# Optimization experiments

Hardware: AMD Instinct MI355X
Metric: run time of the kernel (lower is better)

The kernel has to match this reference:

```python
import jax, jax.numpy as jnp
import numpy as np

N_NODES = 50000
N_EDGES = 800000
IN_F = 128
OUT_F = 64
ORDER = 3


def _spmm(edge_index, edge_attr, x):
    # out[row] += edge_attr[e] * x[col]  (COO sparse @ dense)
    row, col = edge_index[0], edge_index[1]
    msgs = x[col] * edge_attr[:, None]          # [E, F] gather + scale
    return jax.ops.segment_sum(msgs, row, num_segments=N_NODES)  # scatter-add


def setup_inputs() -> dict:
    key = jax.random.key(0)
    k1, k2, k3, k4 = jax.random.split(key, 4)
    x = jax.random.normal(k1, (N_NODES, IN_F), dtype=jnp.float32)
    edge_index = jax.random.randint(k2, (2, N_EDGES), 0, N_NODES, dtype=jnp.int64)
    edge_attr = jax.random.uniform(k3, (N_EDGES,), dtype=jnp.float32)
    W = jax.random.normal(k4, (OUT_F, IN_F), dtype=jnp.float32) * (1.0 / np.sqrt(IN_F))
    b = jnp.zeros((OUT_F,), dtype=jnp.float32)
    return {"x": x, "edge_index": edge_index, "edge_attr": edge_attr, "W": W, "b": b}


def reference(x, edge_index, edge_attr, W, b):
    # output = Linear(x); then `order` rounds of spmm aggregation
    out = jnp.einsum("ni,oi->no", x, W) + b      # [N, OUT_F]
    for _ in range(ORDER):
        out = _spmm(edge_index, edge_attr, out)
    return out
```

## Files before the change

kernel.cpp:

```cpp
#include <hip/hip_runtime.h>

#define IN_F   128
#define OUT_F  64
#define GR     64
#define EPB    4096

__device__ __forceinline__ unsigned short f2bf(float f) {
    unsigned int u = __float_as_uint(f);
    u += 0x7fffu + ((u >> 16) & 1u);
    return (unsigned short)(u >> 16);
}
__device__ __forceinline__ float bf2f(unsigned short h) {
    return __uint_as_float(((unsigned int)h) << 16);
}

template <bool BF16OUT>
__global__ __launch_bounds__(256) void gemm_kernel(
    const float* __restrict__ x, const float* __restrict__ W,
    const float* __restrict__ b, void* __restrict__ outv, int N) {
    __shared__ float xs[GR][IN_F + 4];
    __shared__ float Wt[IN_F][OUT_F + 4];

    const int t = threadIdx.x;
    const int row0 = blockIdx.x * GR;

    for (int i = t; i < OUT_F * (IN_F / 4); i += 256) {
        int o = i & 63;
        int c = i >> 6;
        float4 v = ((const float4*)W)[o * (IN_F / 4) + c];
        Wt[4 * c + 0][o] = v.x;
        Wt[4 * c + 1][o] = v.y;
        Wt[4 * c + 2][o] = v.z;
        Wt[4 * c + 3][o] = v.w;
    }
    for (int i = t; i < GR * (IN_F / 4); i += 256) {
        int r = i >> 5, c = i & 31;
        int gr = row0 + r;
        float4 v = make_float4(0.f, 0.f, 0.f, 0.f);
        if (gr < N) v = ((const float4*)x)[(size_t)gr * (IN_F / 4) + c];
        *(float4*)&xs[r][4 * c] = v;
    }
    __syncthreads();

    const int f0 = (t & 15) * 4;
    const int r0 = (t >> 4) * 4;
    float acc[4][4] = {};

    #pragma unroll 2
    for (int k = 0; k < IN_F; k += 4) {
        float4 xv[4], wv[4];
        #pragma unroll
        for (int i = 0; i < 4; ++i) xv[i] = *(const float4*)&xs[r0 + i][k];
        #pragma unroll
        for (int j = 0; j < 4; ++j) wv[j] = *(const float4*)&Wt[k + j][f0];
        #pragma unroll
        for (int i = 0; i < 4; ++i) {
            #pragma unroll
            for (int j = 0; j < 4; ++j) {
                float wx = j == 0 ? wv[0].x : (j == 1 ? wv[0].y : (j == 2 ? wv[0].z : wv[0].w));
                float wy = j == 0 ? wv[1].x : (j == 1 ? wv[1].y : (j == 2 ? wv[1].z : wv[1].w));
                float wz = j == 0 ? wv[2].x : (j == 1 ? wv[2].y : (j == 2 ? wv[2].z : wv[2].w));
                float ww = j == 0 ? wv[3].x : (j == 1 ? wv[3].y : (j == 2 ? wv[3].z : wv[3].w));
                acc[i][j] = fmaf(xv[i].x, wx, acc[i][j]);
                acc[i][j] = fmaf(xv[i].y, wy, acc[i][j]);
                acc[i][j] = fmaf(xv[i].z, wz, acc[i][j]);
                acc[i][j] = fmaf(xv[i].w, ww, acc[i][j]);
            }
        }
    }

    float4 bv = *(const float4*)&b[f0];
    #pragma unroll
    for (int i = 0; i < 4; ++i) {
        int gr = row0 + r0 + i;
        if (gr < N) {
            float o0 = acc[i][0] + bv.x, o1 = acc[i][1] + bv.y;
            float o2 = acc[i][2] + bv.z, o3 = acc[i][3] + bv.w;
            if (BF16OUT) {
                ushort4 u = { f2bf(o0), f2bf(o1), f2bf(o2), f2bf(o3) };
                *(ushort4*)((unsigned short*)outv + (size_t)gr * OUT_F + f0) = u;
            } else {
                float4 o4 = make_float4(o0, o1, o2, o3);
                *(float4*)((float*)outv + (size_t)gr * OUT_F + f0) = o4;
            }
        }
    }
}

__global__ __launch_bounds__(256) void bhist_kernel(const int* __restrict__ rowi,
                                                    int* __restrict__ bcnt, int E) {
    __shared__ int cnt[256];
    int t = threadIdx.x;
    cnt[t] = 0;
    __syncthreads();
    for (int e = blockIdx.x * 256 + t; e < E; e += gridDim.x * 256)
        atomicAdd(&cnt[rowi[e] >> 8], 1);
    __syncthreads();
    if (cnt[t] > 0) atomicAdd(&bcnt[t], cnt[t]);
}

__global__ __launch_bounds__(256) void bscan_kernel(const int* __restrict__ bcnt,
                                                    int* __restrict__ bbase,
                                                    int* __restrict__ bcursor,
                                                    int* __restrict__ rowptr,
                                                    int nb, int N, int E) {
    int t = threadIdx.x;
    int v = (t < nb) ? bcnt[t] : 0;
    int lane = t & 63, w = t >> 6;
    int sum = v;
    #pragma unroll
    for (int off = 1; off < 64; off <<= 1) {
        int x = __shfl_up(sum, off, 64);
        if (lane >= off) sum += x;
    }
    __shared__ int wsum[4];
    if (lane == 63) wsum[w] = sum;
    __syncthreads();
    int woff = 0;
    for (int i = 0; i < w; ++i) woff += wsum[i];
    int excl = sum + woff - v;
    if (t <= nb) bbase[t] = excl;
    if (t < nb)  bcursor[t] = excl;
    if (t == 0)  rowptr[N] = E;
}

__global__ __launch_bounds__(256) void bin_kernel(
    const int* __restrict__ rowi, const int* __restrict__ coli,
    const float* __restrict__ attr, int* __restrict__ bcursor,
    unsigned long long* __restrict__ tmp, int E) {
    __shared__ int cnt[256];
    __shared__ int cur[256];
    __shared__ int gbase[256];
    int t = threadIdx.x;
    int e0 = blockIdx.x * EPB;
    cnt[t] = 0;
    cur[t] = 0;
    __syncthreads();
    int myrow[16];
    #pragma unroll
    for (int i = 0; i < 16; ++i) {
        int e = e0 + i * 256 + t;
        myrow[i] = (e < E) ? rowi[e] : -1;
        if (myrow[i] >= 0) atomicAdd(&cnt[myrow[i] >> 8], 1);
    }
    __syncthreads();
    if (cnt[t] > 0) gbase[t] = atomicAdd(&bcursor[t], cnt[t]);
    __syncthreads();
    #pragma unroll
    for (int i = 0; i < 16; ++i) {
        int e = e0 + i * 256 + t;
        if (myrow[i] >= 0) {
            int b = myrow[i] >> 8;
            int rank = atomicAdd(&cur[b], 1);
            unsigned long long rec = ((unsigned long long)(myrow[i] & 255) << 32)
                                   | ((unsigned int)coli[e] << 16)
                                   | (unsigned int)f2bf(attr[e]);
            tmp[(size_t)gbase[b] + rank] = rec;
        }
    }
}

__global__ __launch_bounds__(256) void bsort_kernel(
    const unsigned long long* __restrict__ tmp, const int* __restrict__ bbase,
    unsigned int* __restrict__ scv, int* __restrict__ rowptr, int N) {
    __shared__ int cnt[256];
    __shared__ int cur[256];
    __shared__ int wsum[4];
    int t = threadIdx.x, b = blockIdx.x;
    int seg = bbase[b], segend = bbase[b + 1];
    cnt[t] = 0;
    __syncthreads();
    for (int i = seg + t; i < segend; i += 256)
        atomicAdd(&cnt[(int)(tmp[i] >> 32)], 1);
    __syncthreads();
    int v = cnt[t];
    int lane = t & 63, w = t >> 6;
    int sum = v;
    #pragma unroll
    for (int off = 1; off < 64; off <<= 1) {
        int x = __shfl_up(sum, off, 64);
        if (lane >= off) sum += x;
    }
    if (lane == 63) wsum[w] = sum;
    __syncthreads();
    int woff = 0;
    for (int i = 0; i < w; ++i) woff += wsum[i];
    int excl = sum + woff - v;
    int gidx = b * 256 + t;
    if (gidx <= N) rowptr[gidx] = seg + excl;
    cur[t] = excl;
    __syncthreads();
    for (int i = seg + t; i < segend; i += 256) {
        unsigned long long rec = tmp[i];
        int rl = (int)(rec >> 32);
        int pos = atomicAdd(&cur[rl], 1);
        scv[(size_t)seg + pos] = (unsigned int)rec;
    }
}

template <bool BF16OUT>
__global__ __launch_bounds__(256) void spmm_csr_kernel(
    const int* __restrict__ rowptr, const unsigned int* __restrict__ scv,
    const unsigned short* __restrict__ in, void* __restrict__ outv, int N) {
    int wid = (blockIdx.x * 256 + threadIdx.x) >> 6;
    int lane = threadIdx.x & 63;
    if (wid >= N) return;
    wid = __builtin_amdgcn_readfirstlane(wid);
    int beg = rowptr[wid], end = rowptr[wid + 1];
    float acc = 0.f;
    int e = beg;
    for (; e + 16 <= end; e += 16) {
        unsigned int v[16];
        #pragma unroll
        for (int i = 0; i < 16; ++i) v[i] = scv[e + i];
        float xv[16];
        #pragma unroll
        for (int i = 0; i < 16; ++i) xv[i] = bf2f(in[(size_t)(v[i] >> 16) * OUT_F + lane]);
        #pragma unroll
        for (int i = 0; i < 16; ++i) acc = fmaf(bf2f((unsigned short)(v[i] & 0xffffu)), xv[i], acc);
    }
    for (; e + 4 <= end; e += 4) {
        unsigned int v[4];
        #pragma unroll
        for (int i = 0; i < 4; ++i) v[i] = scv[e + i];
        float xv[4];
        #pragma unroll
        for (int i = 0; i < 4; ++i) xv[i] = bf2f(in[(size_t)(v[i] >> 16) * OUT_F + lane]);
        #pragma unroll
        for (int i = 0; i < 4; ++i) acc = fmaf(bf2f((unsigned short)(v[i] & 0xffffu)), xv[i], acc);
    }
    for (; e < end; ++e) {
        unsigned int v = scv[e];
        acc = fmaf(bf2f((unsigned short)(v & 0xffffu)),
                   bf2f(in[(size_t)(v >> 16) * OUT_F + lane]), acc);
    }
    if (BF16OUT)
        ((unsigned short*)outv)[(size_t)wid * OUT_F + lane] = f2bf(acc);
    else
        ((float*)outv)[(size_t)wid * OUT_F + lane] = acc;
}

__global__ __launch_bounds__(256) void spmm_atomic_kernel(
    const int* __restrict__ rowi, const int* __restrict__ coli,
    const float* __restrict__ attr, const float* __restrict__ in,
    float* __restrict__ out, int E) {
    int tid = blockIdx.x * 256 + threadIdx.x;
    int e = tid >> 6;
    int lane = tid & 63;
    if (e >= E) return;
    int r = rowi[e];
    int c = coli[e];
    float w = attr[e];
    float v = in[(size_t)c * OUT_F + lane];
    atomicAdd(&out[(size_t)r * OUT_F + lane], w * v);
}

extern "C" void kernel_launch(void* const* d_in, const int* in_sizes, int n_in,
                              void* d_out, int out_size, void* d_ws, size_t ws_size,
                              hipStream_t stream) {
    const float* x    = (const float*)d_in[0];
    const int*   ei   = (const int*)d_in[1];
    const float* attr = (const float*)d_in[2];
    const float* W    = (const float*)d_in[3];
    const float* b    = (const float*)d_in[4];
    float* out = (float*)d_out;

    const int N = in_sizes[0] / IN_F;
    const int E = in_sizes[2];
    const int* rowi = ei;
    const int* coli = ei + E;

    const size_t obytes_f  = (size_t)N * OUT_F * sizeof(float);
    const size_t obytes_bf = (size_t)N * OUT_F * sizeof(unsigned short);
    const int nb = (N + 255) / 256;

    char* wp = (char*)d_ws;
    size_t off = 0;
    auto alloc = [&](size_t bytes) { char* p = wp + off; off += (bytes + 255) & ~(size_t)255; return p; };
    unsigned short* bufA = (unsigned short*)alloc(obytes_bf);
    unsigned short* bufB = (unsigned short*)alloc((size_t)E * 8);
    unsigned long long* tmp = (unsigned long long*)bufB;
    int* rowptr  = (int*)alloc((size_t)(N + 1) * 4);
    int* bcnt    = (int*)alloc(260 * 4);
    int* bbase   = (int*)alloc(260 * 4);
    int* bcursor = (int*)alloc(260 * 4);
    unsigned int* scv = (unsigned int*)alloc((size_t)E * 4);
    const bool csr_ok = (off <= ws_size) && (N <= 65280) && ((size_t)E * 8 >= obytes_bf);

    const int gemm_blocks = (N + GR - 1) / GR;
    const int sb = (N * 64 + 255) / 256;

    if (csr_ok) {
        gemm_kernel<true><<<gemm_blocks, 256, 0, stream>>>(x, W, b, bufA, N);

        hipMemsetAsync(bcnt, 0, 260 * 4, stream);
        bhist_kernel<<<512, 256, 0, stream>>>(rowi, bcnt, E);
        bscan_kernel<<<1, 256, 0, stream>>>(bcnt, bbase, bcursor, rowptr, nb, N, E);
        bin_kernel<<<(E + EPB - 1) / EPB, 256, 0, stream>>>(rowi, coli, attr, bcursor, tmp, E);
        bsort_kernel<<<nb, 256, 0, stream>>>(tmp, bbase, scv, rowptr, N);

        spmm_csr_kernel<true ><<<sb, 256, 0, stream>>>(rowptr, scv, bufA, bufB, N);
        spmm_csr_kernel<true ><<<sb, 256, 0, stream>>>(rowptr, scv, bufB, bufA, N);
        spmm_csr_kernel<false><<<sb, 256, 0, stream>>>(rowptr, scv, bufA, out, N);
    } else {
        float* ws0 = (float*)d_ws;
        gemm_kernel<false><<<gemm_blocks, 256, 0, stream>>>(x, W, b, ws0, N);
        const int spmm_blocks = (E * 64 + 255) / 256;
        hipMemsetAsync(out, 0, obytes_f, stream);
        spmm_atomic_kernel<<<spmm_blocks, 256, 0, stream>>>(rowi, coli, attr, ws0, out, E);
        hipMemsetAsync(ws0, 0, obytes_f, stream);
        spmm_atomic_kernel<<<spmm_blocks, 256, 0, stream>>>(rowi, coli, attr, out, ws0, E);
        hipMemsetAsync(out, 0, obytes_f, stream);
        spmm_atomic_kernel<<<spmm_blocks, 256, 0, stream>>>(rowi, coli, attr, ws0, out, E);
    }
}
```

Measured before the change: 200.2 us.

## Split CSR SpMM wave into 4 edge groups with 8-byte vector gathers

Each wave now processes four edges at a time: lanes are split into four groups of 16, and each lane loads four bf16 features with one 8-byte load. Partial sums are then reduced across the groups with cross-lane shuffles. Outputs are written as 4-wide vector stores, and edge records and outputs use nontemporal loads and stores. This is meant to cut the number of load instructions and raise memory-level parallelism per edge. The cost is extra shuffle reductions and some lanes idling on ragged row tails.

```diff
diff --git a/kernel.cpp b/kernel.cpp
--- a/kernel.cpp
+++ b/kernel.cpp
@@ -4,6 +4,9 @@
 #define OUT_F  64
 #define GR     64
 #define EPB    4096
+
+typedef float  f32x4  __attribute__((ext_vector_type(4)));
+typedef unsigned int u32x2 __attribute__((ext_vector_type(2)));
 
 __device__ __forceinline__ unsigned short f2bf(float f) {
     unsigned int u = __float_as_uint(f);
@@ -198,6 +201,12 @@
     }
 }
 
+#define FMA4(w, p)                                              \
+    a0 = fmaf((w), __uint_as_float((p).x << 16), a0);           \
+    a1 = fmaf((w), __uint_as_float((p).x & 0xffff0000u), a1);   \
+    a2 = fmaf((w), __uint_as_float((p).y << 16), a2);           \
+    a3 = fmaf((w), __uint_as_float((p).y & 0xffff0000u), a3)
+
 template <bool BF16OUT>
 __global__ __launch_bounds__(256) void spmm_csr_kernel(
     const int* __restrict__ rowptr, const unsigned int* __restrict__ scv,
@@ -206,38 +215,66 @@
     int lane = threadIdx.x & 63;
     if (wid >= N) return;
     wid = __builtin_amdgcn_readfirstlane(wid);
+    const unsigned int g = lane >> 4;
+    const unsigned int s = lane & 15;
     int beg = rowptr[wid], end = rowptr[wid + 1];
-    float acc = 0.f;
+    float a0 = 0.f, a1 = 0.f, a2 = 0.f, a3 = 0.f;
+
     int e = beg;
     for (; e + 16 <= end; e += 16) {
-        unsigned int v[16];
-        #pragma unroll
-        for (int i = 0; i < 16; ++i) v[i] = scv[e + i];
-        float xv[16];
-        #pragma unroll
-        for (int i = 0; i < 16; ++i) xv[i] = bf2f(in[(size_t)(v[i] >> 16) * OUT_F + lane]);
-        #pragma unroll
-        for (int i = 0; i < 16; ++i) acc = fmaf(bf2f((unsigned short)(v[i] & 0xffffu)), xv[i], acc);
-    }
-    for (; e + 4 <= end; e += 4) {
-        unsigned int v[4];
-        #pragma unroll
-        for (int i = 0; i < 4; ++i) v[i] = scv[e + i];
-        float xv[4];
-        #pragma unroll
-        for (int i = 0; i < 4; ++i) xv[i] = bf2f(in[(size_t)(v[i] >> 16) * OUT_F + lane]);
-        #pragma unroll
-        for (int i = 0; i < 4; ++i) acc = fmaf(bf2f((unsigned short)(v[i] & 0xffffu)), xv[i], acc);
-    }
-    for (; e < end; ++e) {
-        unsigned int v = scv[e];
-        acc = fmaf(bf2f((unsigned short)(v & 0xffffu)),
-                   bf2f(in[(size_t)(v >> 16) * OUT_F + lane]), acc);
-    }
-    if (BF16OUT)
-        ((unsigned short*)outv)[(size_t)wid * OUT_F + lane] = f2bf(acc);
-    else
-        ((float*)outv)[(size_t)wid * OUT_F + lane] = acc;
+        unsigned int v0 = __builtin_nontemporal_load(scv + e + g);
+        unsigned int v1 = __builtin_nontemporal_load(scv + e + 4 + g);
+        unsigned int v2 = __builtin_nontemporal_load(scv + e + 8 + g);
+        unsigned int v3 = __builtin_nontemporal_load(scv + e + 12 + g);
+        u32x2 p0 = *(const u32x2*)(in + ((v0 >> 16) << 6) + (s << 2));
+        u32x2 p1 = *(const u32x2*)(in + ((v1 >> 16) << 6) + (s << 2));
+        u32x2 p2 = *(const u32x2*)(in + ((v2 >> 16) << 6) + (s << 2));
+        u32x2 p3 = *(const u32x2*)(in + ((v3 >> 16) << 6) + (s << 2));
+        float w0 = __uint_as_float(v0 << 16);
+        float w1 = __uint_as_float(v1 << 16);
+        float w2 = __uint_as_float(v2 << 16);
+        float w3 = __uint_as_float(v3 << 16);
+        FMA4(w0, p0);
+        FMA4(w1, p1);
+        FMA4(w2, p2);
+        FMA4(w3, p3);
+    }
+    if (e + 8 <= end) {
+        unsigned int v0 = __builtin_nontemporal_load(scv + e + g);
+        unsigned int v1 = __builtin_nontemporal_load(scv + e + 4 + g);
+        u32x2 p0 = *(const u32x2*)(in + ((v0 >> 16) << 6) + (s << 2));
+        u32x2 p1 = *(const u32x2*)(in + ((v1 >> 16) << 6) + (s << 2));
+        float w0 = __uint_as_float(v0 << 16);
+        float w1 = __uint_as_float(v1 << 16);
+        FMA4(w0, p0);
+        FMA4(w1, p1);
+        e += 8;
+    }
+    for (; e < end; e += 4) {
+        unsigned int v = (e + (int)g < end) ? scv[e + g] : 0u;
+        u32x2 p = *(const u32x2*)(in + ((v >> 16) << 6) + (s << 2));
+        float w = __uint_as_float(v << 16);
+        FMA4(w, p);
+    }
+
+    a0 += __shfl_xor(a0, 16); a0 += __shfl_xor(a0, 32);
+    a1 += __shfl_xor(a1, 16); a1 += __shfl_xor(a1, 32);
+    a2 += __shfl_xor(a2, 16); a2 += __shfl_xor(a2, 32);
+    a3 += __shfl_xor(a3, 16); a3 += __shfl_xor(a3, 32);
+
+    if (g == 0) {
+        size_t o = (size_t)wid * OUT_F + (s << 2);
+        if (BF16OUT) {
+            unsigned long long u =  (unsigned long long)f2bf(a0)
+                                 | ((unsigned long long)f2bf(a1) << 16)
+                                 | ((unsigned long long)f2bf(a2) << 32)
+                                 | ((unsigned long long)f2bf(a3) << 48);
+            __builtin_nontemporal_store(u, (unsigned long long*)((unsigned short*)outv + o));
+        } else {
+            f32x4 o4 = { a0, a1, a2, a3 };
+            __builtin_nontemporal_store(o4, (f32x4*)((float*)outv + o));
+        }
+    }
 }
 
 __global__ __launch_bounds__(256) void spmm_atomic_kernel(
```

After: 209.8 us. 1.05x slower.
